# Optimization experiments

Measured on AMD Instinct MI355X. Metric: run time of the kernel, lower is better.

## Reference

```python
import jax, jax.numpy as jnp
import numpy as np

RADIUS = 0.1
NSAMPLE = 32
EPS = 1e-5


def ball_query(p, radius, k):
    # p: (B,N,3) -> idx: (B,N,k) int32. For each query point, take the first k
    # points (in index order) within `radius`; pad with the first found index.
    B, N, _ = p.shape
    d2 = jnp.sum((p[:, :, None, :] - p[:, None, :, :]) ** 2, axis=-1)  # (B,N,N)
    j = jnp.arange(N, dtype=jnp.int32)
    key = jnp.where(d2 < radius * radius, j[None, None, :], N)  # invalid -> N
    neg_small, _ = jax.lax.top_k(-key, k)  # k smallest keys, ascending
    idx = -neg_small                        # (B,N,k)
    first = idx[..., :1]
    idx = jnp.where(idx == N, first, idx)   # pad missing neighbors with first
    return idx


def conv_bn_relu(f, W, g, b, relu=True):
    # f: (B,Cin,N,K); W: (Cout,Cin) 1x1 conv; BatchNorm2d (training stats) + ReLU
    y = jnp.einsum('oc,bcnk->bonk', W, f)
    mean = jnp.mean(y, axis=(0, 2, 3), keepdims=True)
    var = jnp.var(y, axis=(0, 2, 3), keepdims=True)
    y = (y - mean) * jax.lax.rsqrt(var + EPS)
    y = y * g[None, :, None, None] + b[None, :, None, None]
    return jax.nn.relu(y) if relu else y


def reference(p, x, W1, g1, b1, W2, g2, b2):
    # p: (B,N,3), x: (B,C,N)
    B, N, _ = p.shape
    idx = ball_query(p, RADIUS, NSAMPLE)                    # (B,N,K)
    pj = jax.vmap(lambda pts, ix: pts[ix])(p, idx)          # (B,N,K,3)
    dp = pj - p[:, :, None, :]                              # relative coords
    dp = jnp.transpose(dp, (0, 3, 1, 2))                    # (B,3,N,K)
    xt = jnp.transpose(x, (0, 2, 1))                        # (B,N,C)
    xj = jax.vmap(lambda ft, ix: ft[ix])(xt, idx)           # (B,N,K,C)
    xj = jnp.transpose(xj, (0, 3, 1, 2))                    # (B,C,N,K)
    f = jnp.concatenate([dp, xj], axis=1)                   # (B,3+C,N,K)
    f = conv_bn_relu(f, W1, g1, b1, relu=True)
    f = conv_bn_relu(f, W2, g2, b2, relu=True)              # last_act=True
    return jnp.max(f, axis=-1)                              # (B,Cout,N)


def setup_inputs() -> dict:
    key = jax.random.key(0)
    ks = jax.random.split(key, 4)
    B, N, C = 4, 4096, 32
    Cin, Cout = 3 + C, 64
    return {
        'p': jax.random.uniform(ks[0], (B, N, 3), dtype=jnp.float32),
        'x': jax.random.normal(ks[1], (B, C, N), dtype=jnp.float32),
        'W1': jax.random.normal(ks[2], (Cout, Cin), dtype=jnp.float32) * 0.1,
        'g1': jnp.ones((Cout,), jnp.float32),
        'b1': jnp.zeros((Cout,), jnp.float32),
        'W2': jax.random.normal(ks[3], (Cout, Cout), dtype=jnp.float32) * 0.1,
        'g2': jnp.ones((Cout,), jnp.float32),
        'b2': jnp.zeros((Cout,), jnp.float32),
    }
```

## Files before the change

### kernel.cpp

```cpp
#include <hip/hip_runtime.h>
#include <stdint.h>


#define R2 0.01f
#define INVM (1.0f / 524288.0f)

typedef __bf16 bf16x8 __attribute__((ext_vector_type(8)));
typedef float f32x4 __attribute__((ext_vector_type(4)));

__device__ __forceinline__ uint32_t pack_bf16(float a, float b) {
  uint32_t ua = __float_as_uint(a), ub = __float_as_uint(b);
  ua += 0x7fffu + ((ua >> 16) & 1u);
  ub += 0x7fffu + ((ub >> 16) & 1u);
  return (ua >> 16) | (ub & 0xffff0000u);
}
__device__ __forceinline__ float bf_lo(uint32_t v) { return __uint_as_float(v << 16); }
__device__ __forceinline__ float bf_hi(uint32_t v) { return __uint_as_float(v & 0xffff0000u); }

__device__ __forceinline__ int cell_of(float v) {
  const int c = (int)(v * 10.f);
  return c > 9 ? 9 : c;
}

__global__ __launch_bounds__(1024) void k_front(const float* __restrict__ p,
                                                const float* __restrict__ x,
                                                const float* __restrict__ W1,
                                                const float* __restrict__ W2,
                                                void* __restrict__ u,
                                                float* __restrict__ q,
                                                uint32_t* __restrict__ w2frag,
                                                float* __restrict__ part1b,
                                                float* __restrict__ part2b,
                                                float4* __restrict__ cellpts,
                                                int* __restrict__ cellStart) {
  __shared__ __align__(16) char smraw[61440];
  const int bid = blockIdx.x, tid = threadIdx.x;

  if (bid < 128) {
    float* W1s = (float*)smraw;
    for (int tt = tid; tt < 2240; tt += 1024) {
      const int o = tt / 35, cc = tt - o * 35;
      W1s[(cc << 6) + o] = W1[tt];
    }
    __syncthreads();
    const int t = tid & 255, sb = tid >> 8;
    const int g = (bid << 7) + (sb << 5) + (t & 31);
    const int b = g >> 12, nl = g & 4095;
    const int os = (t >> 5) << 3;
    float f[35];
    const float* pb = p + g * 3;
    f[0] = pb[0]; f[1] = pb[1]; f[2] = pb[2];
    const float* xb = x + (b << 17) + nl;
#pragma unroll
    for (int cc = 0; cc < 32; ++cc) f[3 + cc] = xb[cc << 12];
    float acc[8];
#pragma unroll
    for (int o = 0; o < 8; ++o) acc[o] = 0.f;
#pragma unroll
    for (int cc = 0; cc < 35; ++cc) {
      const float fc = f[cc];
      const float4* wp = (const float4*)(W1s + (cc << 6) + os);
      const float4 w0 = wp[0], w1 = wp[1];
      acc[0] = fmaf(w0.x, fc, acc[0]); acc[1] = fmaf(w0.y, fc, acc[1]);
      acc[2] = fmaf(w0.z, fc, acc[2]); acc[3] = fmaf(w0.w, fc, acc[3]);
      acc[4] = fmaf(w1.x, fc, acc[4]); acc[5] = fmaf(w1.y, fc, acc[5]);
      acc[6] = fmaf(w1.z, fc, acc[6]); acc[7] = fmaf(w1.w, fc, acc[7]);
      if (cc == 2) {
        *(float4*)(q + (g << 6) + os)     = make_float4(acc[0], acc[1], acc[2], acc[3]);
        *(float4*)(q + (g << 6) + os + 4) = make_float4(acc[4], acc[5], acc[6], acc[7]);
      }
    }
    uint4 pk;
    pk.x = pack_bf16(acc[0], acc[1]);
    pk.y = pack_bf16(acc[2], acc[3]);
    pk.z = pack_bf16(acc[4], acc[5]);
    pk.w = pack_bf16(acc[6], acc[7]);
    *(uint4*)((char*)u + ((size_t)g << 7) + (os << 1)) = pk;
    return;
  }

  if (bid == 128) {
    for (int tt = tid; tt < 2048; tt += 1024) {
      const int e2 = tt & 3, lane = (tt >> 2) & 63, frag = tt >> 8;
      const int kt = frag >> 2, ot = frag & 3;
      const int c0 = kt * 32 + ((lane >> 4) << 3) + e2 * 2;
      const int o = ot * 16 + (lane & 15);
      w2frag[tt] = pack_bf16(W2[(o << 6) + c0], W2[(o << 6) + c0 + 1]);
    }
    part1b[tid] = 0.f;
    part2b[tid] = 0.f;
    return;
  }

  float* px = (float*)smraw;
  float* py = px + 4096;
  float* pz = py + 4096;
  int* cnt_s = (int*)(smraw + 49152);
  int* scanA = (int*)(smraw + 53248);
  int* scanB = (int*)(smraw + 57344);
  const int b = bid - 129;
  const float* pb = p + b * 12288;
  cnt_s[tid] = 0;
  for (int i = tid; i < 4096; i += 1024) {
    px[i] = pb[3 * i]; py[i] = pb[3 * i + 1]; pz[i] = pb[3 * i + 2];
  }
  __syncthreads();
  for (int i = tid; i < 4096; i += 1024) {
    const int c = (cell_of(px[i]) * 10 + cell_of(py[i])) * 10 + cell_of(pz[i]);
    atomicAdd(&cnt_s[c], 1);
  }
  __syncthreads();
  int* src = scanA; int* dst = scanB;
  src[tid] = cnt_s[tid];
  __syncthreads();
  for (int d = 1; d < 1024; d <<= 1) {
    int v = src[tid];
    if (tid >= d) v += src[tid - d];
    dst[tid] = v;
    __syncthreads();
    int* tmp = src; src = dst; dst = tmp;
  }
  const int excl = (tid == 0) ? 0 : src[tid - 1];
  if (tid <= 1000) cellStart[b * 1001 + tid] = (tid < 1000) ? excl : src[999];
  cnt_s[tid] = excl;
  __syncthreads();
  for (int i = tid; i < 4096; i += 1024) {
    const float xx = px[i], yy = py[i], zz = pz[i];
    const int c = (cell_of(xx) * 10 + cell_of(yy)) * 10 + cell_of(zz);
    const int pos = atomicAdd(&cnt_s[c], 1);
    cellpts[(b << 12) + pos] = make_float4(xx, yy, zz, __int_as_float(i));
  }
}

__global__ __launch_bounds__(256) void k_query(const float* __restrict__ p,
                                               const float4* __restrict__ cellpts,
                                               const int* __restrict__ cellStart,
                                               int* __restrict__ idx) {
  __shared__ uint32_t bm[4][128];
  const int tid = threadIdx.x, w = tid >> 6, lane = tid & 63;
  const int blk0 = blockIdx.x;
  const int blkS = ((blk0 & 7) << 9) + (blk0 >> 3);
  const int n = (blkS << 2) + w;
  const int b = n >> 12;
  bm[w][lane] = 0; bm[w][64 + lane] = 0;
  const float qx = p[n * 3], qy = p[n * 3 + 1], qz = p[n * 3 + 2];
  const int cxq = cell_of(qx), cyq = cell_of(qy), czq = cell_of(qz);

  int cnt_l = 0, startG = 0;
  if (lane < 9) {
    const int cx = cxq + lane / 3 - 1;
    const int cy = cyq + lane % 3 - 1;
    if ((unsigned)cx < 10u && (unsigned)cy < 10u) {
      const int zlo = czq > 0 ? czq - 1 : 0;
      const int zhi = czq < 9 ? czq + 1 : 9;
      const int* cs = cellStart + b * 1001 + (cx * 10 + cy) * 10;
      startG = cs[zlo];
      cnt_l = cs[zhi + 1] - startG;
    }
  }
  int incl = cnt_l;
#pragma unroll
  for (int d = 1; d < 64; d <<= 1) { const int t = __shfl_up(incl, d); if (lane >= d) incl += t; }
  const int T = __shfl(incl, 63);
  const int base_l = startG - (incl - cnt_l);

  for (int tb = 0; tb < T; tb += 64) {
    const int t = tb + lane;
    int s = 0;
#pragma unroll
    for (int m = 0; m < 9; ++m) s += (__shfl(incl, m) <= t);
    const int a = __shfl(base_l, s < 9 ? s : 8);
    if (t < T) {
      const float4 cp = cellpts[(b << 12) + a + t];
      const float dx = cp.x - qx, dy = cp.y - qy, dz = cp.z - qz;
      const float d2 = __fadd_rn(__fadd_rn(__fmul_rn(dx, dx), __fmul_rn(dy, dy)),
                                 __fmul_rn(dz, dz));
      if (d2 < R2) {
        const int j = __float_as_int(cp.w);
        atomicOr(&bm[w][j >> 5], 1u << (j & 31));
      }
    }
  }
  __threadfence_block();

  const uint2 wp2 = *(const uint2*)&bm[w][2 * lane];
  unsigned long long wd = ((unsigned long long)wp2.y << 32) | wp2.x;
  const int pc = __popcll(wd);
  int ip = pc;
#pragma unroll
  for (int d = 1; d < 64; d <<= 1) { const int t = __shfl_up(ip, d); if (lane >= d) ip += t; }
  const int cntT = __shfl(ip, 63);
  int bpos = ip - pc;
  const unsigned long long nz = __ballot(wd != 0ull);
  const int fl = (int)__builtin_ctzll(nz);
  const int fv = wd ? ((lane << 6) + (int)__builtin_ctzll(wd)) : 0;
  const int first = __shfl(fv, fl);
  int* row = idx + (n << 5);
  unsigned long long ww = wd;
  while (ww && bpos < 32) {
    const int j = (lane << 6) + (int)__builtin_ctzll(ww);
    row[bpos] = j;
    ++bpos;
    ww &= ww - 1;
  }
  for (int s = cntT + lane; s < 32; s += 64) row[s] = first;
}

__global__ __launch_bounds__(256) void k_bn1(const void* __restrict__ u,
                                             const float* __restrict__ q,
                                             const int* __restrict__ idx,
                                             float* __restrict__ part1b) {
  __shared__ int idxs[512];
  __shared__ __align__(16) float qs[1024];
  __shared__ float red[8][64];
  const int tid = threadIdx.x;
  const int blk0 = blockIdx.x;
  const int blkS = ((blk0 & 7) << 7) + (blk0 >> 3);
  const int p0 = blkS << 4;
  const int bb = (p0 >> 12) << 12;
  idxs[tid] = idx[(p0 << 5) + tid];
  idxs[256 + tid] = idx[(p0 << 5) + 256 + tid];
#pragma unroll
  for (int i = 0; i < 4; ++i) qs[(i << 8) + tid] = q[(p0 << 6) + (i << 8) + tid];
  __syncthreads();
  const int c4 = tid & 3;
  const char* ub = (const char*)u;
  float s1[16], s2[16];
#pragma unroll
  for (int i = 0; i < 16; ++i) { s1[i] = 0.f; s2[i] = 0.f; }
#pragma unroll 2
  for (int pass = 0; pass < 8; ++pass) {
    const int r = (pass << 6) + (tid >> 2);
    const int j = idxs[r];
    const int pt = r >> 5;
    const uint4* up = (const uint4*)(ub + ((size_t)(bb + j) << 7) + (c4 << 5));
    const uint4 u0 = up[0], u1 = up[1];
    const float* qp = qs + (pt << 6) + (c4 << 4);
    const uint32_t uw[8] = {u0.x, u0.y, u0.z, u0.w, u1.x, u1.y, u1.z, u1.w};
#pragma unroll
    for (int e = 0; e < 8; ++e) {
      const float y0 = bf_lo(uw[e]) - qp[2 * e];
      const float y1 = bf_hi(uw[e]) - qp[2 * e + 1];
      s1[2 * e] += y0;     s2[2 * e] = fmaf(y0, y0, s2[2 * e]);
      s1[2 * e + 1] += y1; s2[2 * e + 1] = fmaf(y1, y1, s2[2 * e + 1]);
    }
  }
#pragma unroll
  for (int i = 0; i < 16; ++i) {
#pragma unroll
    for (int d = 4; d <= 32; d <<= 1) {
      s1[i] += __shfl_xor(s1[i], d);
      s2[i] += __shfl_xor(s2[i], d);
    }
  }
  const int w = tid >> 6, l = tid & 63;
  if (l < 4) {
#pragma unroll
    for (int i = 0; i < 16; ++i) {
      const int ch = (l << 4) + i;
      red[(w << 1)][ch] = s1[i];
      red[(w << 1) + 1][ch] = s2[i];
    }
  }
  __syncthreads();
  if (tid < 128) {
    const int ch = tid & 63, stat = tid >> 6;
    const float v = red[stat][ch] + red[2 + stat][ch] + red[4 + stat][ch] + red[6 + stat][ch];
    atomicAdd(&part1b[((blk0 & 7) << 7) + (stat << 6) + ch], v);
  }
}

__global__ __launch_bounds__(256) void k_stage2(const void* __restrict__ u,
                                                const int* __restrict__ idx,
                                                const float* __restrict__ q,
                                                const float* __restrict__ part1b,
                                                const float* __restrict__ g1,
                                                const float* __restrict__ b1,
                                                const uint32_t* __restrict__ w2frag,
                                                float* __restrict__ part2b,
                                                float* __restrict__ ymax,
                                                float* __restrict__ ymin) {
  __shared__ uint32_t hl[8192];
  __shared__ float rs[8][64];
  __shared__ int   idxs[256];
  __shared__ float ac[128];
  __shared__ float red[8][64];
  const int tid = threadIdx.x, w = tid >> 6, l = tid & 63;
  const int blk0 = blockIdx.x;
  const int blk = ((blk0 & 7) << 8) + (blk0 >> 3);
  const int p0 = blk << 3;
  const int bb = (p0 >> 12) << 12;

  idxs[tid] = idx[(p0 << 5) + tid];
  const float qa = q[(p0 << 6) + tid];
  const float qb = q[(p0 << 6) + 256 + tid];
  if (tid < 64) {
    float s1 = 0.f, s2 = 0.f;
#pragma unroll
    for (int xx = 0; xx < 8; ++xx) {
      s1 += part1b[(xx << 7) + tid];
      s2 += part1b[(xx << 7) + 64 + tid];
    }
    const float mean = s1 * INVM, var = s2 * INVM - mean * mean;
    const float a = g1[tid] * rsqrtf(var + 1e-5f);
    ac[tid] = a; ac[64 + tid] = b1[tid] - mean * a;
  }
  __syncthreads();
  rs[tid >> 6][tid & 63] = fmaf(-ac[tid & 63], qa, ac[64 + (tid & 63)]);
  rs[4 + (tid >> 6)][tid & 63] = fmaf(-ac[tid & 63], qb, ac[64 + (tid & 63)]);
  __syncthreads();

  const int c = tid & 3;
  const char* ub = (const char*)u;
  f32x4 av[4];
#pragma unroll
  for (int k = 0; k < 4; ++k) av[k] = *(const f32x4*)&ac[(c << 4) + (k << 2)];
#pragma unroll
  for (int pass = 0; pass < 4; ++pass) {
    const int r = (pass << 6) + (tid >> 2);
    const int pt = r >> 5;
    const int j = idxs[r];
    const uint4* up = (const uint4*)(ub + ((size_t)(bb + j) << 7) + (c << 5));
    const uint4 u0 = up[0], u1 = up[1];
    f32x4 rv4[4];
#pragma unroll
    for (int k = 0; k < 4; ++k) rv4[k] = *(const f32x4*)&rs[pt][(c << 4) + (k << 2)];
    const uint32_t uw[8] = {u0.x, u0.y, u0.z, u0.w, u1.x, u1.y, u1.z, u1.w};
    uint32_t pk[8];
#pragma unroll
    for (int e = 0; e < 8; ++e) {
      const int i0 = 2 * e, i1 = 2 * e + 1;
      const float h0 = fmaxf(fmaf(av[i0 >> 2][i0 & 3], bf_lo(uw[e]), rv4[i0 >> 2][i0 & 3]), 0.f);
      const float h1 = fmaxf(fmaf(av[i1 >> 2][i1 & 3], bf_hi(uw[e]), rv4[i1 >> 2][i1 & 3]), 0.f);
      pk[e] = pack_bf16(h0, h1);
    }
    const int byte0 = (r << 7) + (c << 5);
    const int sw = (r & 7) << 4;
    *(uint4*)((char*)hl + (byte0 ^ sw)) = make_uint4(pk[0], pk[1], pk[2], pk[3]);
    *(uint4*)((char*)hl + ((byte0 + 16) ^ sw)) = make_uint4(pk[4], pk[5], pk[6], pk[7]);
  }

  bf16x8 bfr[8];
#pragma unroll
  for (int f = 0; f < 8; ++f)
    bfr[f] = __builtin_bit_cast(bf16x8, *(const uint4*)&w2frag[(f << 8) + (l << 2)]);
  __syncthreads();

  float sm_[4] = {0.f, 0.f, 0.f, 0.f}, sq[4] = {0.f, 0.f, 0.f, 0.f};
#pragma unroll 1
  for (int pi = 0; pi < 2; ++pi) {
    const int ptl = (w << 1) + pi;
    const int pn = p0 + ptl;
    float mx[4], mn[4];
#pragma unroll
    for (int ot = 0; ot < 4; ++ot) { mx[ot] = -3e38f; mn[ot] = 3e38f; }
#pragma unroll
    for (int kt2 = 0; kt2 < 2; ++kt2) {
      bf16x8 afr[2];
#pragma unroll
      for (int kt = 0; kt < 2; ++kt) {
        const int srow = (ptl << 5) + (kt2 << 4) + (l & 15);
        int byte = (srow << 7) + (kt << 6) + ((l >> 4) << 4);
        byte ^= (srow & 7) << 4;
        afr[kt] = *(const bf16x8*)((const char*)hl + byte);
      }
#pragma unroll
      for (int ot = 0; ot < 4; ++ot) {
        f32x4 acc = {0.f, 0.f, 0.f, 0.f};
        acc = __builtin_amdgcn_mfma_f32_16x16x32_bf16(afr[0], bfr[ot], acc, 0, 0, 0);
        acc = __builtin_amdgcn_mfma_f32_16x16x32_bf16(afr[1], bfr[4 + ot], acc, 0, 0, 0);
#pragma unroll
        for (int e = 0; e < 4; ++e) {
          const float v = acc[e];
          mx[ot] = fmaxf(mx[ot], v); mn[ot] = fminf(mn[ot], v);
          sm_[ot] += v; sq[ot] = fmaf(v, v, sq[ot]);
        }
      }
    }
#pragma unroll
    for (int ot = 0; ot < 4; ++ot) {
      float a = fmaxf(mx[ot], __shfl_xor(mx[ot], 16)); a = fmaxf(a, __shfl_xor(a, 32));
      float b = fminf(mn[ot], __shfl_xor(mn[ot], 16)); b = fminf(b, __shfl_xor(b, 32));
      const int o = (ot << 4) + (l & 15);
      if (l < 16)      ymax[(pn << 6) + o] = a;
      else if (l < 32) ymin[(pn << 6) + o] = b;
    }
  }
#pragma unroll
  for (int ot = 0; ot < 4; ++ot) {
    float s = sm_[ot]; s += __shfl_xor(s, 16); s += __shfl_xor(s, 32);
    float t2 = sq[ot]; t2 += __shfl_xor(t2, 16); t2 += __shfl_xor(t2, 32);
    if (l < 16) { red[w][(ot << 4) + l] = s; red[4 + w][(ot << 4) + l] = t2; }
  }
  __syncthreads();
  if (tid < 128) {
    const int ch = tid & 63, sel = (tid >= 64) ? 4 : 0;
    const float v = red[sel][ch] + red[sel + 1][ch] + red[sel + 2][ch] + red[sel + 3][ch];
    atomicAdd(&part2b[((blk0 & 7) << 7) + tid], v);
  }
}

__global__ __launch_bounds__(256) void k_out(const float* __restrict__ ymax,
                                             const float* __restrict__ ymin,
                                             const float* __restrict__ part2b,
                                             const float* __restrict__ g2,
                                             const float* __restrict__ b2,
                                             float* __restrict__ out) {
  __shared__ float ac[128];
  __shared__ float tile[64][65];
  const int tid = threadIdx.x;
  if (tid < 64) {
    float s1 = 0.f, s2 = 0.f;
#pragma unroll
    for (int xx = 0; xx < 8; ++xx) {
      s1 += part2b[(xx << 7) + tid];
      s2 += part2b[(xx << 7) + 64 + tid];
    }
    const float mean = s1 * INVM, var = s2 * INVM - mean * mean;
    const float a = g2[tid] * rsqrtf(var + 1e-5f);
    ac[tid] = a; ac[64 + tid] = b2[tid] - mean * a;
  }
  __syncthreads();
  const int b = blockIdx.x >> 6, nt = blockIdx.x & 63;
  const int pnbase = (b << 12) + (nt << 6);
#pragma unroll
  for (int i = 0; i < 16; ++i) {
    const int e = i * 256 + tid;
    const int nl = e >> 6, o = e & 63;
    const float a = ac[o], c = ac[64 + o];
    const int src = ((pnbase + nl) << 6) + o;
    const float v = (a >= 0.f) ? ymax[src] : ymin[src];
    tile[nl][o] = fmaxf(fmaf(a, v, c), 0.f);
  }
  __syncthreads();
#pragma unroll
  for (int i = 0; i < 16; ++i) {
    const int e = i * 256 + tid;
    const int ol = e >> 6, nl = e & 63;
    out[(b << 18) + (ol << 12) + (nt << 6) + nl] = tile[nl][ol];
  }
}

extern "C" void kernel_launch(void* const* d_in, const int* in_sizes, int n_in,
                              void* d_out, int out_size, void* d_ws, size_t ws_size,
                              hipStream_t stream) {
  const float* p  = (const float*)d_in[0];
  const float* x  = (const float*)d_in[1];
  const float* W1 = (const float*)d_in[2];
  const float* g1 = (const float*)d_in[3];
  const float* b1 = (const float*)d_in[4];
  const float* W2 = (const float*)d_in[5];
  const float* g2 = (const float*)d_in[6];
  const float* b2 = (const float*)d_in[7];
  float* out = (float*)d_out;

  char* ws = (char*)d_ws;
  size_t off = 0;
  int* idx        = (int*)(ws + off);      off += 2097152;
  void* u         = (void*)(ws + off);     off += 2097152;
  float* q        = (float*)(ws + off);    off += 4194304;
  uint32_t* w2f   = (uint32_t*)(ws + off); off += 8192;
  float* part1b   = (float*)(ws + off);    off += 4096;
  float* part2b   = (float*)(ws + off);    off += 4096;
  float* ymax     = (float*)(ws + off);    off += 4194304;
  float* ymin     = (float*)(ws + off);    off += 4194304;
  float4* cellpts = (float4*)(ws + off);   off += 262144;
  int* cellStart  = (int*)(ws + off);      off += 16384;

  k_front<<<dim3(133), dim3(1024), 0, stream>>>(p, x, W1, W2, u, q, w2f,
                                                part1b, part2b, cellpts, cellStart);
  k_query<<<dim3(4096), dim3(256), 0, stream>>>(p, cellpts, cellStart, idx);
  k_bn1<<<dim3(1024), dim3(256), 0, stream>>>(u, q, idx, part1b);
  k_stage2<<<dim3(2048), dim3(256), 0, stream>>>(u, idx, q, part1b, g1, b1, w2f,
                                                 part2b, ymax, ymin);
  k_out<<<dim3(256), dim3(256), 0, stream>>>(ymax, ymin, part2b, g2, b2, out);
}
```

Before: 54.73 us.

## Shrink front kernel blocks, wave-scan cell grid, store q term as bf16

The front kernel changes from 133 blocks of 1024 threads to 517 blocks of 256 threads. This spreads the W1 projection over more CUs and cuts shared memory use. The per-batch cell binning now reads points straight from global memory and uses a shuffle-based wave scan over 4-cell chunks instead of a barrier-heavy Hillis-Steele scan. The per-point q term (the coordinate part of the first conv) is stored as packed bf16 instead of fp32, halving its traffic in the producer and both consumers, at some cost in accuracy for the BN1 centering term.

```diff
diff --git a/kernel.cpp b/kernel.cpp
--- a/kernel.cpp
+++ b/kernel.cpp
@@ -22,31 +22,30 @@
   return c > 9 ? 9 : c;
 }
 
-__global__ __launch_bounds__(1024) void k_front(const float* __restrict__ p,
-                                                const float* __restrict__ x,
-                                                const float* __restrict__ W1,
-                                                const float* __restrict__ W2,
-                                                void* __restrict__ u,
-                                                float* __restrict__ q,
-                                                uint32_t* __restrict__ w2frag,
-                                                float* __restrict__ part1b,
-                                                float* __restrict__ part2b,
-                                                float4* __restrict__ cellpts,
-                                                int* __restrict__ cellStart) {
-  __shared__ __align__(16) char smraw[61440];
+__global__ __launch_bounds__(256) void k_front(const float* __restrict__ p,
+                                               const float* __restrict__ x,
+                                               const float* __restrict__ W1,
+                                               const float* __restrict__ W2,
+                                               void* __restrict__ u,
+                                               void* __restrict__ qpk,
+                                               uint32_t* __restrict__ w2frag,
+                                               float* __restrict__ part1b,
+                                               float* __restrict__ part2b,
+                                               float4* __restrict__ cellpts,
+                                               int* __restrict__ cellStart) {
+  __shared__ __align__(16) char smraw[8960];
   const int bid = blockIdx.x, tid = threadIdx.x;
 
-  if (bid < 128) {
+  if (bid < 512) {
     float* W1s = (float*)smraw;
-    for (int tt = tid; tt < 2240; tt += 1024) {
+    for (int tt = tid; tt < 2240; tt += 256) {
       const int o = tt / 35, cc = tt - o * 35;
       W1s[(cc << 6) + o] = W1[tt];
     }
     __syncthreads();
-    const int t = tid & 255, sb = tid >> 8;
-    const int g = (bid << 7) + (sb << 5) + (t & 31);
+    const int g = (bid << 5) + (tid & 31);
     const int b = g >> 12, nl = g & 4095;
-    const int os = (t >> 5) << 3;
+    const int os = (tid >> 5) << 3;
     float f[35];
     const float* pb = p + g * 3;
     f[0] = pb[0]; f[1] = pb[1]; f[2] = pb[2];
@@ -66,70 +65,76 @@
       acc[4] = fmaf(w1.x, fc, acc[4]); acc[5] = fmaf(w1.y, fc, acc[5]);
       acc[6] = fmaf(w1.z, fc, acc[6]); acc[7] = fmaf(w1.w, fc, acc[7]);
       if (cc == 2) {
-        *(float4*)(q + (g << 6) + os)     = make_float4(acc[0], acc[1], acc[2], acc[3]);
-        *(float4*)(q + (g << 6) + os + 4) = make_float4(acc[4], acc[5], acc[6], acc[7]);
+        uint4 qp4;
+        qp4.x = pack_bf16(acc[0], acc[1]); qp4.y = pack_bf16(acc[2], acc[3]);
+        qp4.z = pack_bf16(acc[4], acc[5]); qp4.w = pack_bf16(acc[6], acc[7]);
+        *(uint4*)((char*)qpk + ((size_t)g << 7) + (os << 1)) = qp4;
       }
     }
     uint4 pk;
-    pk.x = pack_bf16(acc[0], acc[1]);
-    pk.y = pack_bf16(acc[2], acc[3]);
-    pk.z = pack_bf16(acc[4], acc[5]);
-    pk.w = pack_bf16(acc[6], acc[7]);
+    pk.x = pack_bf16(acc[0], acc[1]); pk.y = pack_bf16(acc[2], acc[3]);
+    pk.z = pack_bf16(acc[4], acc[5]); pk.w = pack_bf16(acc[6], acc[7]);
     *(uint4*)((char*)u + ((size_t)g << 7) + (os << 1)) = pk;
     return;
   }
 
-  if (bid == 128) {
-    for (int tt = tid; tt < 2048; tt += 1024) {
-      const int e2 = tt & 3, lane = (tt >> 2) & 63, frag = tt >> 8;
-      const int kt = frag >> 2, ot = frag & 3;
-      const int c0 = kt * 32 + ((lane >> 4) << 3) + e2 * 2;
-      const int o = ot * 16 + (lane & 15);
-      w2frag[tt] = pack_bf16(W2[(o << 6) + c0], W2[(o << 6) + c0 + 1]);
-    }
-    part1b[tid] = 0.f;
-    part2b[tid] = 0.f;
+  if (bid < 516) {
+    int* cnt_s = (int*)smraw;
+    int* wsum = (int*)(smraw + 4096);
+    const int b = bid - 512;
+    const float* pb = p + b * 12288;
+    for (int i = tid; i < 1024; i += 256) cnt_s[i] = 0;
+    __syncthreads();
+    for (int i = tid; i < 4096; i += 256) {
+      const float xx = pb[3 * i], yy = pb[3 * i + 1], zz = pb[3 * i + 2];
+      const int c = (cell_of(xx) * 10 + cell_of(yy)) * 10 + cell_of(zz);
+      atomicAdd(&cnt_s[c], 1);
+    }
+    __syncthreads();
+    int c0 = 0, c1 = 0, c2 = 0, c3 = 0;
+    if (tid < 250) {
+      c0 = cnt_s[4 * tid]; c1 = cnt_s[4 * tid + 1];
+      c2 = cnt_s[4 * tid + 2]; c3 = cnt_s[4 * tid + 3];
+    }
+    const int chunk = c0 + c1 + c2 + c3;
+    int incl = chunk;
+#pragma unroll
+    for (int d = 1; d < 64; d <<= 1) { const int t = __shfl_up(incl, d); if ((tid & 63) >= d) incl += t; }
+    const int w = tid >> 6, lane = tid & 63;
+    if (lane == 63) wsum[w] = incl;
+    __syncthreads();
+    int wpre = 0;
+    for (int i = 0; i < w; ++i) wpre += wsum[i];
+    const int excl = wpre + incl - chunk;
+    if (tid < 250) {
+      int* cs = cellStart + b * 1001 + 4 * tid;
+      cs[0] = excl;           cs[1] = excl + c0;
+      cs[2] = excl + c0 + c1; cs[3] = excl + c0 + c1 + c2;
+    }
+    if (tid == 0) cellStart[b * 1001 + 1000] = 4096;
+    __syncthreads();
+    if (tid < 250) {
+      cnt_s[4 * tid] = excl;           cnt_s[4 * tid + 1] = excl + c0;
+      cnt_s[4 * tid + 2] = excl + c0 + c1; cnt_s[4 * tid + 3] = excl + c0 + c1 + c2;
+    }
+    __syncthreads();
+    for (int i = tid; i < 4096; i += 256) {
+      const float xx = pb[3 * i], yy = pb[3 * i + 1], zz = pb[3 * i + 2];
+      const int c = (cell_of(xx) * 10 + cell_of(yy)) * 10 + cell_of(zz);
+      const int pos = atomicAdd(&cnt_s[c], 1);
+      cellpts[(b << 12) + pos] = make_float4(xx, yy, zz, __int_as_float(i));
+    }
     return;
   }
 
-  float* px = (float*)smraw;
-  float* py = px + 4096;
-  float* pz = py + 4096;
-  int* cnt_s = (int*)(smraw + 49152);
-  int* scanA = (int*)(smraw + 53248);
-  int* scanB = (int*)(smraw + 57344);
-  const int b = bid - 129;
-  const float* pb = p + b * 12288;
-  cnt_s[tid] = 0;
-  for (int i = tid; i < 4096; i += 1024) {
-    px[i] = pb[3 * i]; py[i] = pb[3 * i + 1]; pz[i] = pb[3 * i + 2];
-  }
-  __syncthreads();
-  for (int i = tid; i < 4096; i += 1024) {
-    const int c = (cell_of(px[i]) * 10 + cell_of(py[i])) * 10 + cell_of(pz[i]);
-    atomicAdd(&cnt_s[c], 1);
-  }
-  __syncthreads();
-  int* src = scanA; int* dst = scanB;
-  src[tid] = cnt_s[tid];
-  __syncthreads();
-  for (int d = 1; d < 1024; d <<= 1) {
-    int v = src[tid];
-    if (tid >= d) v += src[tid - d];
-    dst[tid] = v;
-    __syncthreads();
-    int* tmp = src; src = dst; dst = tmp;
-  }
-  const int excl = (tid == 0) ? 0 : src[tid - 1];
-  if (tid <= 1000) cellStart[b * 1001 + tid] = (tid < 1000) ? excl : src[999];
-  cnt_s[tid] = excl;
-  __syncthreads();
-  for (int i = tid; i < 4096; i += 1024) {
-    const float xx = px[i], yy = py[i], zz = pz[i];
-    const int c = (cell_of(xx) * 10 + cell_of(yy)) * 10 + cell_of(zz);
-    const int pos = atomicAdd(&cnt_s[c], 1);
-    cellpts[(b << 12) + pos] = make_float4(xx, yy, zz, __int_as_float(i));
-  }
+  for (int tt = tid; tt < 2048; tt += 256) {
+    const int e2 = tt & 3, lane = (tt >> 2) & 63, frag = tt >> 8;
+    const int kt = frag >> 2, ot = frag & 3;
+    const int c0 = kt * 32 + ((lane >> 4) << 3) + e2 * 2;
+    const int o = ot * 16 + (lane & 15);
+    w2frag[tt] = pack_bf16(W2[(o << 6) + c0], W2[(o << 6) + c0 + 1]);
+  }
+  for (int i = tid; i < 1024; i += 256) { part1b[i] = 0.f; part2b[i] = 0.f; }
 }
 
 __global__ __launch_bounds__(256) void k_query(const float* __restrict__ p,
@@ -207,7 +212,7 @@
 }
 
 __global__ __launch_bounds__(256) void k_bn1(const void* __restrict__ u,
-                                             const float* __restrict__ q,
+                                             const void* __restrict__ qpk,
                                              const int* __restrict__ idx,
                                              float* __restrict__ part1b) {
   __shared__ int idxs[512];
@@ -220,8 +225,13 @@
   const int bb = (p0 >> 12) << 12;
   idxs[tid] = idx[(p0 << 5) + tid];
   idxs[256 + tid] = idx[(p0 << 5) + 256 + tid];
-#pragma unroll
-  for (int i = 0; i < 4; ++i) qs[(i << 8) + tid] = q[(p0 << 6) + (i << 8) + tid];
+  const uint32_t* qp32 = (const uint32_t*)qpk;
+#pragma unroll
+  for (int i = 0; i < 2; ++i) {
+    const int e = (i << 8) + tid;
+    const uint32_t v = qp32[(p0 << 5) + e];
+    qs[2 * e] = bf_lo(v); qs[2 * e + 1] = bf_hi(v);
+  }
   __syncthreads();
   const int c4 = tid & 3;
   const char* ub = (const char*)u;
@@ -272,7 +282,7 @@
 
 __global__ __launch_bounds__(256) void k_stage2(const void* __restrict__ u,
                                                 const int* __restrict__ idx,
-                                                const float* __restrict__ q,
+                                                const void* __restrict__ qpk,
                                                 const float* __restrict__ part1b,
                                                 const float* __restrict__ g1,
                                                 const float* __restrict__ b1,
@@ -292,8 +302,7 @@
   const int bb = (p0 >> 12) << 12;
 
   idxs[tid] = idx[(p0 << 5) + tid];
-  const float qa = q[(p0 << 6) + tid];
-  const float qb = q[(p0 << 6) + 256 + tid];
+  const uint32_t qw = ((const uint32_t*)qpk)[(p0 << 5) + tid];
   if (tid < 64) {
     float s1 = 0.f, s2 = 0.f;
 #pragma unroll
@@ -306,8 +315,11 @@
     ac[tid] = a; ac[64 + tid] = b1[tid] - mean * a;
   }
   __syncthreads();
-  rs[tid >> 6][tid & 63] = fmaf(-ac[tid & 63], qa, ac[64 + (tid & 63)]);
-  rs[4 + (tid >> 6)][tid & 63] = fmaf(-ac[tid & 63], qb, ac[64 + (tid & 63)]);
+  {
+    const int pt = tid >> 5, pr = tid & 31;
+    rs[pt][2 * pr]     = fmaf(-ac[2 * pr], bf_lo(qw), ac[64 + 2 * pr]);
+    rs[pt][2 * pr + 1] = fmaf(-ac[2 * pr + 1], bf_hi(qw), ac[64 + 2 * pr + 1]);
+  }
   __syncthreads();
 
   const int c = tid & 3;
@@ -325,13 +337,13 @@
     f32x4 rv4[4];
 #pragma unroll
     for (int k = 0; k < 4; ++k) rv4[k] = *(const f32x4*)&rs[pt][(c << 4) + (k << 2)];
-    const uint32_t uw[8] = {u0.x, u0.y, u0.z, u0.w, u1.x, u1.y, u1.z, u1.w};
+    const uint32_t uw8[8] = {u0.x, u0.y, u0.z, u0.w, u1.x, u1.y, u1.z, u1.w};
     uint32_t pk[8];
 #pragma unroll
     for (int e = 0; e < 8; ++e) {
       const int i0 = 2 * e, i1 = 2 * e + 1;
-      const float h0 = fmaxf(fmaf(av[i0 >> 2][i0 & 3], bf_lo(uw[e]), rv4[i0 >> 2][i0 & 3]), 0.f);
-      const float h1 = fmaxf(fmaf(av[i1 >> 2][i1 & 3], bf_hi(uw[e]), rv4[i1 >> 2][i1 & 3]), 0.f);
+      const float h0 = fmaxf(fmaf(av[i0 >> 2][i0 & 3], bf_lo(uw8[e]), rv4[i0 >> 2][i0 & 3]), 0.f);
+      const float h1 = fmaxf(fmaf(av[i1 >> 2][i1 & 3], bf_hi(uw8[e]), rv4[i1 >> 2][i1 & 3]), 0.f);
       pk[e] = pack_bf16(h0, h1);
     }
     const int byte0 = (r << 7) + (c << 5);
@@ -458,7 +470,7 @@
   size_t off = 0;
   int* idx        = (int*)(ws + off);      off += 2097152;
   void* u         = (void*)(ws + off);     off += 2097152;
-  float* q        = (float*)(ws + off);    off += 4194304;
+  void* qpk       = (void*)(ws + off);     off += 2097152;
   uint32_t* w2f   = (uint32_t*)(ws + off); off += 8192;
   float* part1b   = (float*)(ws + off);    off += 4096;
   float* part2b   = (float*)(ws + off);    off += 4096;
@@ -467,11 +479,11 @@
   float4* cellpts = (float4*)(ws + off);   off += 262144;
   int* cellStart  = (int*)(ws + off);      off += 16384;
 
-  k_front<<<dim3(133), dim3(1024), 0, stream>>>(p, x, W1, W2, u, q, w2f,
-                                                part1b, part2b, cellpts, cellStart);
+  k_front<<<dim3(517), dim3(256), 0, stream>>>(p, x, W1, W2, u, qpk, w2f,
+                                               part1b, part2b, cellpts, cellStart);
   k_query<<<dim3(4096), dim3(256), 0, stream>>>(p, cellpts, cellStart, idx);
-  k_bn1<<<dim3(1024), dim3(256), 0, stream>>>(u, q, idx, part1b);
-  k_stage2<<<dim3(2048), dim3(256), 0, stream>>>(u, idx, q, part1b, g1, b1, w2f,
+  k_bn1<<<dim3(1024), dim3(256), 0, stream>>>(u, qpk, idx, part1b);
+  k_stage2<<<dim3(2048), dim3(256), 0, stream>>>(u, idx, qpk, part1b, g1, b1, w2f,
                                                  part2b, ymax, ymin);
   k_out<<<dim3(256), dim3(256), 0, stream>>>(ymax, ymin, part2b, g2, b2, out);
 }
```

Result: slower. 57.38 us (+4.8%).
